# Optimization experiments

Measured on AMD Instinct MI355X. Metric: run time of the kernel, lower is better.

Reference implementation:

```python
import jax, jax.numpy as jnp
import numpy as np

B, S, D, H = 2, 2048, 2048, 16
HD = D // H  # 128 head dim


def setup_inputs() -> dict:
    key = jax.random.key(0)
    k1, k2, k3 = jax.random.split(key, 3)
    x = jax.random.normal(k1, (B, S, D), dtype=jnp.float32)
    w_qkv = jax.random.normal(k2, (3 * D, D), dtype=jnp.float32) * 0.02
    w_out = jax.random.normal(k3, (D, D), dtype=jnp.float32) * 0.02
    # complex-like RoPE table: freqs_cis[s, j] = exp(i * s * theta^{-2j/hd})
    theta = 10000.0
    inv_freq = 1.0 / (theta ** (jnp.arange(0, HD, 2, dtype=jnp.float32) / HD))  # [HD/2]
    t = jnp.arange(S, dtype=jnp.float32)
    freqs = jnp.outer(t, inv_freq)  # [S, HD/2]
    return {"x": x, "w_qkv": w_qkv, "w_out": w_out,
            "freqs_cos": jnp.cos(freqs), "freqs_sin": jnp.sin(freqs)}


def _apply_rope(t, cos, sin):
    # t: [b, s, h, hd]; adjacent pairs treated as complex (real, imag)
    b, s, h, hd = t.shape
    tr = t.reshape(b, s, h, hd // 2, 2)
    re, im = tr[..., 0], tr[..., 1]
    c = cos[None, :, None, :]  # [1, s, 1, hd/2]
    sn = sin[None, :, None, :]
    out_re = re * c - im * sn
    out_im = re * sn + im * c
    return jnp.stack([out_re, out_im], axis=-1).reshape(b, s, h, hd)


def reference(x, w_qkv, w_out, freqs_cos, freqs_sin):
    b, s, d = x.shape
    qkv = x @ w_qkv.T  # [b, s, 3d]
    q, k, v = jnp.split(qkv, 3, axis=-1)
    q = q.reshape(b, s, H, HD)
    k = k.reshape(b, s, H, HD)
    v = v.reshape(b, s, H, HD)
    q = _apply_rope(q, freqs_cos, freqs_sin)
    k = _apply_rope(k, freqs_cos, freqs_sin)
    # causal SDPA
    scale = 1.0 / jnp.sqrt(jnp.asarray(HD, dtype=x.dtype))
    scores = jnp.einsum("bqhd,bkhd->bhqk", q, k) * scale  # [b, h, s, s]
    causal = jnp.tril(jnp.ones((s, s), dtype=bool))
    scores = jnp.where(causal[None, None], scores, jnp.finfo(scores.dtype).min)
    attn = jax.nn.softmax(scores, axis=-1)
    out = jnp.einsum("bhqk,bkhd->bqhd", attn, v).reshape(b, s, d)
    return out @ w_out.T
```

## Files before the change

kernel.cpp:

```cpp
#include <hip/hip_runtime.h>
#include <hip/hip_bf16.h>
#include <stdint.h>

#define S_ 2048
#define D_ 2048
#define H_ 16
#define HD_ 128

typedef __bf16 bf16x8 __attribute__((ext_vector_type(8)));
typedef float f32x4 __attribute__((ext_vector_type(4)));
typedef unsigned short ushort_t;
typedef ushort_t us4 __attribute__((ext_vector_type(4)));

__device__ __forceinline__ float bf2f(ushort_t u) {
  union { float f; uint32_t i; } x; x.i = ((uint32_t)u) << 16; return x.f;
}
__device__ __forceinline__ ushort_t f2bf(float f) {
  union { float f; uint32_t i; } x; x.f = f;
  uint32_t r = x.i + 0x7fffu + ((x.i >> 16) & 1u);
  return (ushort_t)(r >> 16);
}

__device__ __forceinline__ void async_copy16(const void* g, void* l) {
  __builtin_amdgcn_global_load_lds(
      (const __attribute__((address_space(1))) unsigned int*)g,
      (__attribute__((address_space(3))) unsigned int*)l, 16, 0, 0);
}

__device__ __forceinline__ void store_val(float* p, float v) { *p = v; }
__device__ __forceinline__ void store_val(ushort_t* p, float v) { *p = f2bf(v); }

__global__ __launch_bounds__(256) void cvt_f32_bf16(const float* __restrict__ in,
                                                    ushort_t* __restrict__ out,
                                                    int n4) {
  int i = blockIdx.x * 256 + threadIdx.x;
  if (i >= n4) return;
  const float4 v = ((const float4*)in)[i];
  us4 o;
  o.x = f2bf(v.x); o.y = f2bf(v.y); o.z = f2bf(v.z); o.w = f2bf(v.w);
  ((us4*)out)[i] = o;
}

template <typename OutT>
__global__ __launch_bounds__(256) void gemm_bt(const ushort_t* __restrict__ A,
                                               const ushort_t* __restrict__ Bm,
                                               OutT* __restrict__ C,
                                               int M, int N, int K) {
  __shared__ __align__(16) ushort_t As[128 * 32];
  __shared__ __align__(16) ushort_t Bs[128 * 32];
  const int tid = threadIdx.x;
  const int wave = tid >> 6, lane = tid & 63;
  const int quad = lane >> 4, l16 = lane & 15;
  const int bm = blockIdx.y * 128, bn = blockIdx.x * 128;
  const int wm = (wave >> 1) * 64, wn = (wave & 1) * 64;

  f32x4 acc[4][4] = {};

  const int c0 = wave * 2, c1 = c0 + 1;
  const int srow = lane >> 2;
  const int scol = (lane & 3) * 8;
  const ushort_t* gA0 = A + (size_t)(bm + c0 * 16 + srow) * K + scol;
  const ushort_t* gA1 = A + (size_t)(bm + c1 * 16 + srow) * K + scol;
  const ushort_t* gB0 = Bm + (size_t)(bn + c0 * 16 + srow) * K + scol;
  const ushort_t* gB1 = Bm + (size_t)(bn + c1 * 16 + srow) * K + scol;
  ushort_t* lA0 = As + c0 * 512;
  ushort_t* lA1 = As + c1 * 512;
  ushort_t* lB0 = Bs + c0 * 512;
  ushort_t* lB1 = Bs + c1 * 512;

  for (int k0 = 0; k0 < K; k0 += 32) {
    __syncthreads();
    async_copy16(gA0 + k0, lA0);
    async_copy16(gA1 + k0, lA1);
    async_copy16(gB0 + k0, lB0);
    async_copy16(gB1 + k0, lB1);
    __syncthreads();
    bf16x8 af[4], bfr[4];
#pragma unroll
    for (int i = 0; i < 4; ++i)
      af[i] = *(const bf16x8*)(As + (wm + i * 16 + l16) * 32 + quad * 8);
#pragma unroll
    for (int i = 0; i < 4; ++i)
      bfr[i] = *(const bf16x8*)(Bs + (wn + i * 16 + l16) * 32 + quad * 8);
#pragma unroll
    for (int mi = 0; mi < 4; ++mi)
#pragma unroll
      for (int ni = 0; ni < 4; ++ni)
        acc[mi][ni] = __builtin_amdgcn_mfma_f32_16x16x32_bf16(af[mi], bfr[ni],
                                                              acc[mi][ni], 0, 0, 0);
  }
#pragma unroll
  for (int mi = 0; mi < 4; ++mi)
#pragma unroll
    for (int ni = 0; ni < 4; ++ni)
#pragma unroll
      for (int r = 0; r < 4; ++r) {
        int row = bm + wm + mi * 16 + quad * 4 + r;
        int col = bn + wn + ni * 16 + l16;
        store_val(&C[(size_t)row * N + col], acc[mi][ni][r]);
      }
}

__global__ __launch_bounds__(256) void rope_k(ushort_t* __restrict__ qkv,
                                              const float* __restrict__ fc,
                                              const float* __restrict__ fs) {
  int idx = blockIdx.x * 256 + threadIdx.x;
  int i = idx & 63;
  int hh = (idx >> 6) & 15;
  int m = idx >> 10;
  int s = m & (S_ - 1);
  float c = fc[s * 64 + i], sn = fs[s * 64 + i];
  size_t off = (size_t)m * (3 * D_) + hh * HD_ + 2 * i;
#pragma unroll
  for (int part = 0; part < 2; ++part) {
    uint32_t* p = (uint32_t*)(qkv + off + part * D_);
    uint32_t v = *p;
    float re = bf2f((ushort_t)(v & 0xffffu));
    float im = bf2f((ushort_t)(v >> 16));
    float nr = re * c - im * sn;
    float ni = re * sn + im * c;
    *p = (uint32_t)f2bf(nr) | ((uint32_t)f2bf(ni) << 16);
  }
}

__global__ __launch_bounds__(256) void vt_prep(const ushort_t* __restrict__ qkv,
                                               ushort_t* __restrict__ VTg) {
  __shared__ __align__(16) ushort_t T[64 * 136];
  const int st = blockIdx.x, h = blockIdx.y, b = blockIdx.z;
  const int tid = threadIdx.x;
  const ushort_t* gV = qkv + (size_t)(b * S_ + st * 64) * (3 * D_) + 2 * D_ + h * HD_;
  {
    const int r = tid >> 2, cc = (tid & 3) * 32;
    const ushort_t* src = gV + (size_t)r * (3 * D_) + cc;
    uint4 a0 = ((const uint4*)src)[0];
    uint4 a1 = ((const uint4*)src)[1];
    uint4 a2 = ((const uint4*)src)[2];
    uint4 a3 = ((const uint4*)src)[3];
    ushort_t* dst = T + r * 136 + cc;
    ((uint4*)dst)[0] = a0; ((uint4*)dst)[1] = a1;
    ((uint4*)dst)[2] = a2; ((uint4*)dst)[3] = a3;
  }
  __syncthreads();
  const int d = tid >> 1, kh = (tid & 1) * 32;
  ushort_t buf[32];
#pragma unroll
  for (int j = 0; j < 32; ++j) buf[j] = T[(kh + j) * 136 + d];
  ushort_t* out = VTg + ((size_t)((b * H_ + h) * HD_ + d)) * S_ + st * 64 + kh;
  ((uint4*)out)[0] = *(const uint4*)(buf + 0);
  ((uint4*)out)[1] = *(const uint4*)(buf + 8);
  ((uint4*)out)[2] = *(const uint4*)(buf + 16);
  ((uint4*)out)[3] = *(const uint4*)(buf + 24);
}

#define SOFTMAX_C 12.0f

__global__ __launch_bounds__(256, 4) void attn_fwd(const ushort_t* __restrict__ qkv,
                                                   const ushort_t* __restrict__ VTg,
                                                   float* __restrict__ Oacc,
                                                   float* __restrict__ lsum_g) {
  __shared__ __align__(16) ushort_t Kl[64 * 128];
  __shared__ __align__(16) ushort_t VT[128 * 64];
  __shared__ __align__(16) ushort_t Pl[4 * 16 * 64];

  const int j = 79 - (int)blockIdx.x;
  int qt, c;
  if (j < 8)       { qt = j;                 c = 0; }
  else if (j < 24) { int t = j - 8;  qt = 8 + (t >> 1);  c = t & 1; }
  else if (j < 48) { int t = j - 24; qt = 16 + t / 3;    c = t % 3; }
  else             { int t = j - 48; qt = 24 + (t >> 2); c = t & 3; }
  const int h = blockIdx.y, b = blockIdx.z;
  const int kt0 = c * 8;
  const int kt_end = min(kt0 + 8, qt + 1);

  const int tid = threadIdx.x;
  const int wave = tid >> 6, lane = tid & 63;
  const int quad = lane >> 4, l16 = lane & 15;
  const float scale = 0.08838834764831845f;

  const int qg = qt * 64 + wave * 16 + l16;
  const ushort_t* qrow = qkv + (size_t)(b * S_ + qg) * (3 * D_) + h * HD_;
  bf16x8 qf[4];
#pragma unroll
  for (int cc = 0; cc < 4; ++cc)
    qf[cc] = *(const bf16x8*)(qrow + cc * 32 + quad * 8);

  f32x4 o[8] = {};
  float lsum[4] = {0.f, 0.f, 0.f, 0.f};
  const int q_row_base = qt * 64 + wave * 16 + quad * 4;
  ushort_t* Pw = Pl + wave * 16 * 64;

  const ushort_t* gK = qkv + (size_t)(b * S_) * (3 * D_) + D_ + h * HD_;
  const ushort_t* gVT = VTg + (size_t)(b * H_ + h) * HD_ * S_;

  const int krow_off = lane >> 4;
  const int kchunk = lane & 15;
  const int vrow_off = lane >> 3;
  const int vchunk = lane & 7;

  for (int kt = kt0; kt < kt_end; ++kt) {
    __syncthreads();
#pragma unroll
    for (int i = 0; i < 4; ++i) {
      int row = wave * 16 + i * 4 + krow_off;
      int lchunk = kchunk ^ (row & 15);
      async_copy16(gK + (size_t)(kt * 64 + row) * (3 * D_) + lchunk * 8,
                   Kl + (wave * 16 + i * 4) * 128);
    }
#pragma unroll
    for (int i = 0; i < 4; ++i) {
      int row = wave * 32 + i * 8 + vrow_off;
      int lchunk = vchunk ^ (row & 7);
      async_copy16(gVT + (size_t)row * S_ + kt * 64 + lchunk * 8,
                   VT + (wave * 32 + i * 8) * 64);
    }
    __syncthreads();

    const bool diag = (kt == qt);
#pragma unroll
    for (int g = 0; g < 4; ++g) {
      f32x4 s = {0.f, 0.f, 0.f, 0.f};
#pragma unroll
      for (int cc = 0; cc < 4; ++cc) {
        bf16x8 kf = *(const bf16x8*)(Kl + (g * 16 + l16) * 128 +
                                     (((cc * 4 + quad) ^ l16) * 8));
        s = __builtin_amdgcn_mfma_f32_16x16x32_bf16(qf[cc], kf, s, 0, 0, 0);
      }
      const int key = kt * 64 + g * 16 + l16;
#pragma unroll
      for (int r = 0; r < 4; ++r) {
        float e = __expf(s[r] * scale - SOFTMAX_C);
        float p = (!diag || key <= q_row_base + r) ? e : 0.f;
        lsum[r] += p;
        int prow = quad * 4 + r;
        int pcol = g * 16 + l16;
        Pw[prow * 64 + (((pcol >> 3) ^ (prow & 7)) * 8) + (pcol & 7)] = f2bf(p);
      }
    }
    bf16x8 pf0 = *(const bf16x8*)(Pw + l16 * 64 + ((quad ^ (l16 & 7)) * 8));
    bf16x8 pf1 = *(const bf16x8*)(Pw + l16 * 64 + (((4 + quad) ^ (l16 & 7)) * 8));
#pragma unroll
    for (int dc = 0; dc < 8; ++dc) {
      bf16x8 v0 = *(const bf16x8*)(VT + (dc * 16 + l16) * 64 +
                                   (((0 * 4 + quad) ^ (l16 & 7)) * 8));
      o[dc] = __builtin_amdgcn_mfma_f32_16x16x32_bf16(pf0, v0, o[dc], 0, 0, 0);
      bf16x8 v1 = *(const bf16x8*)(VT + (dc * 16 + l16) * 64 +
                                   (((1 * 4 + quad) ^ (l16 & 7)) * 8));
      o[dc] = __builtin_amdgcn_mfma_f32_16x16x32_bf16(pf1, v1, o[dc], 0, 0, 0);
    }
  }

#pragma unroll
  for (int r = 0; r < 4; ++r) {
    float l = lsum[r];
    l += __shfl_xor(l, 1, 64);
    l += __shfl_xor(l, 2, 64);
    l += __shfl_xor(l, 4, 64);
    l += __shfl_xor(l, 8, 64);
    size_t row = (size_t)(b * S_ + q_row_base + r);
    if (l16 == 0) unsafeAtomicAdd(&lsum_g[row * H_ + h], l);
#pragma unroll
    for (int dc = 0; dc < 8; ++dc)
      unsafeAtomicAdd(&Oacc[row * D_ + h * HD_ + dc * 16 + l16], o[dc][r]);
  }
}

__global__ __launch_bounds__(256) void combine(const float* __restrict__ Oacc,
                                               const float* __restrict__ lsum_g,
                                               ushort_t* __restrict__ attn) {
  int i = blockIdx.x * 256 + threadIdx.x;
  float4 v = ((const float4*)Oacc)[i];
  int flat = i * 4;
  int row = flat >> 11;
  int h = (flat >> 7) & 15;
  float inv = 1.0f / lsum_g[row * H_ + h];
  us4 o;
  o.x = f2bf(v.x * inv); o.y = f2bf(v.y * inv);
  o.z = f2bf(v.z * inv); o.w = f2bf(v.w * inv);
  ((us4*)attn)[i] = o;
}

extern "C" void kernel_launch(void* const* d_in, const int* in_sizes, int n_in,
                              void* d_out, int out_size, void* d_ws, size_t ws_size,
                              hipStream_t stream) {
  const float* x = (const float*)d_in[0];
  const float* w_qkv = (const float*)d_in[1];
  const float* w_out = (const float*)d_in[2];
  const float* fcos = (const float*)d_in[3];
  const float* fsin = (const float*)d_in[4];
  float* out = (float*)d_out;

  char* ws = (char*)d_ws;
  ushort_t* x_bf    = (ushort_t*)(ws + 0);
  ushort_t* wqkv_bf = (ushort_t*)(ws + 16777216);
  ushort_t* wout_bf = (ushort_t*)(ws + 41943040);
  ushort_t* qkv     = (ushort_t*)(ws + 50331648);
  ushort_t* attn    = (ushort_t*)(ws + 100663296);
  float* Oacc   = (float*)(ws + 0);
  float* lsum_g = (float*)(ws + 33554432);
  ushort_t* VTg = (ushort_t*)(ws + 100663296);

  cvt_f32_bf16<<<8192, 256, 0, stream>>>(x, x_bf, 2097152);
  cvt_f32_bf16<<<12288, 256, 0, stream>>>(w_qkv, wqkv_bf, 3145728);
  cvt_f32_bf16<<<4096, 256, 0, stream>>>(w_out, wout_bf, 1048576);

  gemm_bt<ushort_t><<<dim3(48, 32), 256, 0, stream>>>(x_bf, wqkv_bf, qkv,
                                                      4096, 6144, 2048);
  rope_k<<<16384, 256, 0, stream>>>(qkv, fcos, fsin);
  vt_prep<<<dim3(32, 16, 2), 256, 0, stream>>>(qkv, VTg);

  hipMemsetAsync(Oacc, 0, 33554432, stream);
  hipMemsetAsync(lsum_g, 0, 262144, stream);

  attn_fwd<<<dim3(80, 16, 2), 256, 0, stream>>>(qkv, VTg, Oacc, lsum_g);
  combine<<<8192, 256, 0, stream>>>(Oacc, lsum_g, attn);

  gemm_bt<float><<<dim3(16, 32), 256, 0, stream>>>(attn, wout_bf, out,
                                                   4096, 2048, 2048);
}
```

Baseline: 461.7 us.

## Pad GEMM LDS tiles against bank conflicts and split-K the output projection

The GEMM shared-memory tiles get a row stride of 40 elements instead of 32, with the async-copy mapping rewritten (5 slots per row, the fifth a dummy) to reduce LDS bank conflicts on fragment reads. The output projection GEMM now splits K in two across blockIdx.z and accumulates into the output with float atomics. This doubles the block count on a grid of only 512 tiles. The cost is a memset of the output, atomic traffic, and some wasted copy slots for padding.

```diff
diff --git a/kernel.cpp b/kernel.cpp
--- a/kernel.cpp
+++ b/kernel.cpp
@@ -41,47 +41,54 @@
   ((us4*)out)[i] = o;
 }
 
-template <typename OutT>
+#define GPAD 40
+template <typename OutT, bool ATOMIC>
 __global__ __launch_bounds__(256) void gemm_bt(const ushort_t* __restrict__ A,
                                                const ushort_t* __restrict__ Bm,
                                                OutT* __restrict__ C,
-                                               int M, int N, int K) {
-  __shared__ __align__(16) ushort_t As[128 * 32];
-  __shared__ __align__(16) ushort_t Bs[128 * 32];
+                                               int M, int N, int K, int ksplit) {
+  __shared__ __align__(16) ushort_t As[128 * GPAD + 256];
+  __shared__ __align__(16) ushort_t Bs[128 * GPAD + 256];
   const int tid = threadIdx.x;
   const int wave = tid >> 6, lane = tid & 63;
   const int quad = lane >> 4, l16 = lane & 15;
   const int bm = blockIdx.y * 128, bn = blockIdx.x * 128;
   const int wm = (wave >> 1) * 64, wn = (wave & 1) * 64;
+  const int kbeg = blockIdx.z * ksplit, kend = kbeg + ksplit;
 
   f32x4 acc[4][4] = {};
 
-  const int c0 = wave * 2, c1 = c0 + 1;
-  const int srow = lane >> 2;
-  const int scol = (lane & 3) * 8;
-  const ushort_t* gA0 = A + (size_t)(bm + c0 * 16 + srow) * K + scol;
-  const ushort_t* gA1 = A + (size_t)(bm + c1 * 16 + srow) * K + scol;
-  const ushort_t* gB0 = Bm + (size_t)(bn + c0 * 16 + srow) * K + scol;
-  const ushort_t* gB1 = Bm + (size_t)(bn + c1 * 16 + srow) * K + scol;
-  ushort_t* lA0 = As + c0 * 512;
-  ushort_t* lA1 = As + c1 * 512;
-  ushort_t* lB0 = Bs + c0 * 512;
-  ushort_t* lB1 = Bs + c1 * 512;
-
-  for (int k0 = 0; k0 < K; k0 += 32) {
+  const int w160 = wave * 160;
+  const ushort_t* gAp[3];
+  const ushort_t* gBp[3];
+  ushort_t* ldsA[3];
+  ushort_t* ldsB[3];
+#pragma unroll
+  for (int i = 0; i < 3; ++i) {
+    int s = w160 + i * 64 + lane;
+    int r = s / 5, c = s % 5;
+    if (r > 127) r = 127;
+    int sc = (c == 4) ? 0 : c;
+    gAp[i] = A + (size_t)(bm + r) * K + sc * 8;
+    gBp[i] = Bm + (size_t)(bn + r) * K + sc * 8;
+    ldsA[i] = As + (w160 + i * 64) * 8;
+    ldsB[i] = Bs + (w160 + i * 64) * 8;
+  }
+
+  for (int k0 = kbeg; k0 < kend; k0 += 32) {
     __syncthreads();
-    async_copy16(gA0 + k0, lA0);
-    async_copy16(gA1 + k0, lA1);
-    async_copy16(gB0 + k0, lB0);
-    async_copy16(gB1 + k0, lB1);
+#pragma unroll
+    for (int i = 0; i < 3; ++i) async_copy16(gAp[i] + k0, ldsA[i]);
+#pragma unroll
+    for (int i = 0; i < 3; ++i) async_copy16(gBp[i] + k0, ldsB[i]);
     __syncthreads();
     bf16x8 af[4], bfr[4];
 #pragma unroll
     for (int i = 0; i < 4; ++i)
-      af[i] = *(const bf16x8*)(As + (wm + i * 16 + l16) * 32 + quad * 8);
+      af[i] = *(const bf16x8*)(As + (wm + i * 16 + l16) * GPAD + quad * 8);
 #pragma unroll
     for (int i = 0; i < 4; ++i)
-      bfr[i] = *(const bf16x8*)(Bs + (wn + i * 16 + l16) * 32 + quad * 8);
+      bfr[i] = *(const bf16x8*)(Bs + (wn + i * 16 + l16) * GPAD + quad * 8);
 #pragma unroll
     for (int mi = 0; mi < 4; ++mi)
 #pragma unroll
@@ -97,7 +104,10 @@
       for (int r = 0; r < 4; ++r) {
         int row = bm + wm + mi * 16 + quad * 4 + r;
         int col = bn + wn + ni * 16 + l16;
-        store_val(&C[(size_t)row * N + col], acc[mi][ni][r]);
+        if constexpr (ATOMIC)
+          unsafeAtomicAdd((float*)&C[(size_t)row * N + col], acc[mi][ni][r]);
+        else
+          store_val(&C[(size_t)row * N + col], acc[mi][ni][r]);
       }
 }
 
@@ -299,12 +309,14 @@
   float* lsum_g = (float*)(ws + 33554432);
   ushort_t* VTg = (ushort_t*)(ws + 100663296);
 
+  hipMemsetAsync(out, 0, 33554432, stream);
+
   cvt_f32_bf16<<<8192, 256, 0, stream>>>(x, x_bf, 2097152);
   cvt_f32_bf16<<<12288, 256, 0, stream>>>(w_qkv, wqkv_bf, 3145728);
   cvt_f32_bf16<<<4096, 256, 0, stream>>>(w_out, wout_bf, 1048576);
 
-  gemm_bt<ushort_t><<<dim3(48, 32), 256, 0, stream>>>(x_bf, wqkv_bf, qkv,
-                                                      4096, 6144, 2048);
+  gemm_bt<ushort_t, false><<<dim3(48, 32, 1), 256, 0, stream>>>(
+      x_bf, wqkv_bf, qkv, 4096, 6144, 2048, 2048);
   rope_k<<<16384, 256, 0, stream>>>(qkv, fcos, fsin);
   vt_prep<<<dim3(32, 16, 2), 256, 0, stream>>>(qkv, VTg);
 
@@ -314,6 +326,6 @@
   attn_fwd<<<dim3(80, 16, 2), 256, 0, stream>>>(qkv, VTg, Oacc, lsum_g);
   combine<<<8192, 256, 0, stream>>>(Oacc, lsum_g, attn);
 
-  gemm_bt<float><<<dim3(16, 32), 256, 0, stream>>>(attn, wout_bf, out,
-                                                   4096, 2048, 2048);
-}
+  gemm_bt<float, true><<<dim3(16, 32, 2), 256, 0, stream>>>(
+      attn, wout_bf, out, 4096, 2048, 2048, 1024);
+}
```

Measured after the change: 519.3 us. +12.5%, slower.

## Fuse conversions, fold RoPE into QKV GEMM epilogue, split-K output projection

Applied to the files above, without the earlier changes.

The three fp32-to-bf16 conversion launches become one kernel writing into the contiguous workspace. RoPE moves into the QKV GEMM epilogue, using a lane shuffle to pair real and imaginary columns, which removes a separate read-modify-write pass over Q and K. The output projection is split over K into two slices that accumulate with float atomics into a zeroed output, doubling the block count from 512 to 1024 in exchange for a memset and atomic traffic. RoPE is now applied to the fp32 accumulator before bf16 rounding, which changes rounding slightly.

```diff
diff --git a/kernel.cpp b/kernel.cpp
--- a/kernel.cpp
+++ b/kernel.cpp
@@ -30,22 +30,26 @@
 __device__ __forceinline__ void store_val(float* p, float v) { *p = v; }
 __device__ __forceinline__ void store_val(ushort_t* p, float v) { *p = f2bf(v); }
 
-__global__ __launch_bounds__(256) void cvt_f32_bf16(const float* __restrict__ in,
-                                                    ushort_t* __restrict__ out,
-                                                    int n4) {
+__global__ __launch_bounds__(256) void cvt_all(const float* __restrict__ x,
+                                               const float* __restrict__ wqkv,
+                                               const float* __restrict__ wout,
+                                               ushort_t* __restrict__ dst) {
   int i = blockIdx.x * 256 + threadIdx.x;
-  if (i >= n4) return;
-  const float4 v = ((const float4*)in)[i];
+  const float4 v = (i < 2097152) ? ((const float4*)x)[i]
+                 : (i < 5242880) ? ((const float4*)wqkv)[i - 2097152]
+                                 : ((const float4*)wout)[i - 5242880];
   us4 o;
   o.x = f2bf(v.x); o.y = f2bf(v.y); o.z = f2bf(v.z); o.w = f2bf(v.w);
-  ((us4*)out)[i] = o;
-}
-
-template <typename OutT>
+  ((us4*)dst)[i] = o;
+}
+
+template <typename OutT, bool ATOMIC, bool ROPE>
 __global__ __launch_bounds__(256) void gemm_bt(const ushort_t* __restrict__ A,
                                                const ushort_t* __restrict__ Bm,
                                                OutT* __restrict__ C,
-                                               int M, int N, int K) {
+                                               int M, int N, int K, int ksplit,
+                                               const float* __restrict__ fc,
+                                               const float* __restrict__ fs) {
   __shared__ __align__(16) ushort_t As[128 * 32];
   __shared__ __align__(16) ushort_t Bs[128 * 32];
   const int tid = threadIdx.x;
@@ -53,6 +57,7 @@
   const int quad = lane >> 4, l16 = lane & 15;
   const int bm = blockIdx.y * 128, bn = blockIdx.x * 128;
   const int wm = (wave >> 1) * 64, wn = (wave & 1) * 64;
+  const int kbeg = blockIdx.z * ksplit, kend = kbeg + ksplit;
 
   f32x4 acc[4][4] = {};
 
@@ -68,7 +73,7 @@
   ushort_t* lB0 = Bs + c0 * 512;
   ushort_t* lB1 = Bs + c1 * 512;
 
-  for (int k0 = 0; k0 < K; k0 += 32) {
+  for (int k0 = kbeg; k0 < kend; k0 += 32) {
     __syncthreads();
     async_copy16(gA0 + k0, lA0);
     async_copy16(gA1 + k0, lA1);
@@ -89,38 +94,31 @@
         acc[mi][ni] = __builtin_amdgcn_mfma_f32_16x16x32_bf16(af[mi], bfr[ni],
                                                               acc[mi][ni], 0, 0, 0);
   }
+  const bool do_rope = ROPE && (bn < 2 * D_);
 #pragma unroll
   for (int mi = 0; mi < 4; ++mi)
 #pragma unroll
-    for (int ni = 0; ni < 4; ++ni)
+    for (int ni = 0; ni < 4; ++ni) {
+      const int col = bn + wn + ni * 16 + l16;
 #pragma unroll
       for (int r = 0; r < 4; ++r) {
-        int row = bm + wm + mi * 16 + quad * 4 + r;
-        int col = bn + wn + ni * 16 + l16;
-        store_val(&C[(size_t)row * N + col], acc[mi][ni][r]);
+        const int row = bm + wm + mi * 16 + quad * 4 + r;
+        float v = acc[mi][ni][r];
+        if (do_rope) {
+          const int s = row & (S_ - 1);
+          const int fi = (col >> 1) & 63;
+          const float c = fc[s * 64 + fi];
+          const float sn = fs[s * 64 + fi];
+          const float other = __shfl_xor(v, 1, 64);
+          v = (col & 1) ? (other * sn + v * c)
+                        : (v * c - other * sn);
+        }
+        if constexpr (ATOMIC)
+          unsafeAtomicAdd((float*)&C[(size_t)row * N + col], v);
+        else
+          store_val(&C[(size_t)row * N + col], v);
       }
-}
-
-__global__ __launch_bounds__(256) void rope_k(ushort_t* __restrict__ qkv,
-                                              const float* __restrict__ fc,
-                                              const float* __restrict__ fs) {
-  int idx = blockIdx.x * 256 + threadIdx.x;
-  int i = idx & 63;
-  int hh = (idx >> 6) & 15;
-  int m = idx >> 10;
-  int s = m & (S_ - 1);
-  float c = fc[s * 64 + i], sn = fs[s * 64 + i];
-  size_t off = (size_t)m * (3 * D_) + hh * HD_ + 2 * i;
-#pragma unroll
-  for (int part = 0; part < 2; ++part) {
-    uint32_t* p = (uint32_t*)(qkv + off + part * D_);
-    uint32_t v = *p;
-    float re = bf2f((ushort_t)(v & 0xffffu));
-    float im = bf2f((ushort_t)(v >> 16));
-    float nr = re * c - im * sn;
-    float ni = re * sn + im * c;
-    *p = (uint32_t)f2bf(nr) | ((uint32_t)f2bf(ni) << 16);
-  }
+    }
 }
 
 __global__ __launch_bounds__(256) void vt_prep(const ushort_t* __restrict__ qkv,
@@ -299,13 +297,13 @@
   float* lsum_g = (float*)(ws + 33554432);
   ushort_t* VTg = (ushort_t*)(ws + 100663296);
 
-  cvt_f32_bf16<<<8192, 256, 0, stream>>>(x, x_bf, 2097152);
-  cvt_f32_bf16<<<12288, 256, 0, stream>>>(w_qkv, wqkv_bf, 3145728);
-  cvt_f32_bf16<<<4096, 256, 0, stream>>>(w_out, wout_bf, 1048576);
-
-  gemm_bt<ushort_t><<<dim3(48, 32), 256, 0, stream>>>(x_bf, wqkv_bf, qkv,
-                                                      4096, 6144, 2048);
-  rope_k<<<16384, 256, 0, stream>>>(qkv, fcos, fsin);
+  hipMemsetAsync(out, 0, 33554432, stream);
+
+  cvt_all<<<24576, 256, 0, stream>>>(x, w_qkv, w_out, x_bf);
+
+  gemm_bt<ushort_t, false, true><<<dim3(48, 32, 1), 256, 0, stream>>>(
+      x_bf, wqkv_bf, qkv, 4096, 6144, 2048, 2048, fcos, fsin);
+
   vt_prep<<<dim3(32, 16, 2), 256, 0, stream>>>(qkv, VTg);
 
   hipMemsetAsync(Oacc, 0, 33554432, stream);
@@ -314,6 +312,6 @@
   attn_fwd<<<dim3(80, 16, 2), 256, 0, stream>>>(qkv, VTg, Oacc, lsum_g);
   combine<<<8192, 256, 0, stream>>>(Oacc, lsum_g, attn);
 
-  gemm_bt<float><<<dim3(16, 32), 256, 0, stream>>>(attn, wout_bf, out,
-                                                   4096, 2048, 2048);
-}
+  gemm_bt<float, true, false><<<dim3(16, 32, 2), 256, 0, stream>>>(
+      attn, wout_bf, out, 4096, 2048, 2048, 1024, nullptr, nullptr);
+}
```

Result: slower. 515.9 us (+11.7%).

## Fuse input conversions into one kernel and split-K the output projection

Applied to the files above, without the earlier changes.

The three fp32-to-bf16 conversion launches are merged into a single kernel that picks its source by index, which relies on x_bf, wqkv_bf and wout_bf sitting contiguously in the workspace. The output projection GEMM, which launched only 512 blocks, is split along K into two halves that accumulate into the fp32 output with atomic adds after the output is zeroed by a memset. This is meant to raise occupancy on a GPU with many compute units and to cut launch overhead. In exchange it adds a 32MB memset, doubles the atomic write traffic, and makes the summation order nondeterministic.

```diff
diff --git a/kernel.cpp b/kernel.cpp
--- a/kernel.cpp
+++ b/kernel.cpp
@@ -30,22 +30,24 @@
 __device__ __forceinline__ void store_val(float* p, float v) { *p = v; }
 __device__ __forceinline__ void store_val(ushort_t* p, float v) { *p = f2bf(v); }
 
-__global__ __launch_bounds__(256) void cvt_f32_bf16(const float* __restrict__ in,
-                                                    ushort_t* __restrict__ out,
-                                                    int n4) {
+__global__ __launch_bounds__(256) void cvt_all(const float* __restrict__ x,
+                                               const float* __restrict__ wqkv,
+                                               const float* __restrict__ wout,
+                                               ushort_t* __restrict__ dst) {
   int i = blockIdx.x * 256 + threadIdx.x;
-  if (i >= n4) return;
-  const float4 v = ((const float4*)in)[i];
+  const float4 v = (i < 2097152) ? ((const float4*)x)[i]
+                 : (i < 5242880) ? ((const float4*)wqkv)[i - 2097152]
+                                 : ((const float4*)wout)[i - 5242880];
   us4 o;
   o.x = f2bf(v.x); o.y = f2bf(v.y); o.z = f2bf(v.z); o.w = f2bf(v.w);
-  ((us4*)out)[i] = o;
-}
-
-template <typename OutT>
+  ((us4*)dst)[i] = o;
+}
+
+template <typename OutT, bool ATOMIC>
 __global__ __launch_bounds__(256) void gemm_bt(const ushort_t* __restrict__ A,
                                                const ushort_t* __restrict__ Bm,
                                                OutT* __restrict__ C,
-                                               int M, int N, int K) {
+                                               int M, int N, int K, int ksplit) {
   __shared__ __align__(16) ushort_t As[128 * 32];
   __shared__ __align__(16) ushort_t Bs[128 * 32];
   const int tid = threadIdx.x;
@@ -53,6 +55,7 @@
   const int quad = lane >> 4, l16 = lane & 15;
   const int bm = blockIdx.y * 128, bn = blockIdx.x * 128;
   const int wm = (wave >> 1) * 64, wn = (wave & 1) * 64;
+  const int kbeg = blockIdx.z * ksplit, kend = kbeg + ksplit;
 
   f32x4 acc[4][4] = {};
 
@@ -68,7 +71,7 @@
   ushort_t* lB0 = Bs + c0 * 512;
   ushort_t* lB1 = Bs + c1 * 512;
 
-  for (int k0 = 0; k0 < K; k0 += 32) {
+  for (int k0 = kbeg; k0 < kend; k0 += 32) {
     __syncthreads();
     async_copy16(gA0 + k0, lA0);
     async_copy16(gA1 + k0, lA1);
@@ -97,7 +100,10 @@
       for (int r = 0; r < 4; ++r) {
         int row = bm + wm + mi * 16 + quad * 4 + r;
         int col = bn + wn + ni * 16 + l16;
-        store_val(&C[(size_t)row * N + col], acc[mi][ni][r]);
+        if constexpr (ATOMIC)
+          unsafeAtomicAdd((float*)&C[(size_t)row * N + col], acc[mi][ni][r]);
+        else
+          store_val(&C[(size_t)row * N + col], acc[mi][ni][r]);
       }
 }
 
@@ -299,12 +305,13 @@
   float* lsum_g = (float*)(ws + 33554432);
   ushort_t* VTg = (ushort_t*)(ws + 100663296);
 
-  cvt_f32_bf16<<<8192, 256, 0, stream>>>(x, x_bf, 2097152);
-  cvt_f32_bf16<<<12288, 256, 0, stream>>>(w_qkv, wqkv_bf, 3145728);
-  cvt_f32_bf16<<<4096, 256, 0, stream>>>(w_out, wout_bf, 1048576);
-
-  gemm_bt<ushort_t><<<dim3(48, 32), 256, 0, stream>>>(x_bf, wqkv_bf, qkv,
-                                                      4096, 6144, 2048);
+  hipMemsetAsync(out, 0, 33554432, stream);
+
+  cvt_all<<<24576, 256, 0, stream>>>(x, w_qkv, w_out, x_bf);
+
+  gemm_bt<ushort_t, false><<<dim3(48, 32, 1), 256, 0, stream>>>(
+      x_bf, wqkv_bf, qkv, 4096, 6144, 2048, 2048);
+
   rope_k<<<16384, 256, 0, stream>>>(qkv, fcos, fsin);
   vt_prep<<<dim3(32, 16, 2), 256, 0, stream>>>(qkv, VTg);
 
@@ -314,6 +321,6 @@
   attn_fwd<<<dim3(80, 16, 2), 256, 0, stream>>>(qkv, VTg, Oacc, lsum_g);
   combine<<<8192, 256, 0, stream>>>(Oacc, lsum_g, attn);
 
-  gemm_bt<float><<<dim3(16, 32), 256, 0, stream>>>(attn, wout_bf, out,
-                                                   4096, 2048, 2048);
-}
+  gemm_bt<float, true><<<dim3(16, 32, 2), 256, 0, stream>>>(
+      attn, wout_bf, out, 4096, 2048, 2048, 1024);
+}
```

Result: slower. 498.4 us (+8.0%).
